# Kernel tuning notes

Measured on AMD Instinct MI355X. Metric: run time of the kernel, lower is better.

The kernel has to match this reference:

```python
import jax, jax.numpy as jnp
import numpy as np

EPS = 1e-5

def layer_norm(x, g, b):
    mu = jnp.mean(x, axis=-1, keepdims=True)
    var = jnp.var(x, axis=-1, keepdims=True)
    return (x - mu) * jax.lax.rsqrt(var + EPS) * g + b

def rel_shift(x):
    # x: [N, H, T1, T2] with T2 = 2*T1 - 1 -> [N, H, T1, T1]
    N, H, T1, T2 = x.shape
    zp = jnp.zeros((N, H, T1, 1), dtype=x.dtype)
    xp = jnp.concatenate([zp, x], axis=-1).reshape(N, H, T2 + 1, T1)
    x = xp[:, :, 1:, :].reshape(N, H, T1, T2)
    return x[:, :, :, : T2 // 2 + 1]

def setup_inputs() -> dict:
    B, T, D, Hh = 8, 1024, 512, 8
    dk = D // Hh
    P = 2 * T - 1
    key = jax.random.key(0)
    ks = jax.random.split(key, 12)
    s = 0.02
    return {
        "q": jax.random.normal(ks[0], (B, T, D), jnp.float32),
        "k": jax.random.normal(ks[1], (B, T, D), jnp.float32),
        "v": jax.random.normal(ks[2], (B, T, D), jnp.float32),
        "pos_emb": jax.random.normal(ks[3], (1, P, D), jnp.float32),
        "mask": jnp.ones((B, T, T), jnp.int32),
        "ln_q_g": jnp.ones((D,), jnp.float32), "ln_q_b": jnp.zeros((D,), jnp.float32),
        "ln_k_g": jnp.ones((D,), jnp.float32), "ln_k_b": jnp.zeros((D,), jnp.float32),
        "ln_v_g": jnp.ones((D,), jnp.float32), "ln_v_b": jnp.zeros((D,), jnp.float32),
        "w_q": jax.random.normal(ks[4], (D, D), jnp.float32) * s,   # [out, in]
        "w_k": jax.random.normal(ks[5], (D, D), jnp.float32) * s,
        "w_v": jax.random.normal(ks[6], (D, D), jnp.float32) * s,
        "w_pos": jax.random.normal(ks[7], (D, D), jnp.float32) * s,
        "w_fc": jax.random.normal(ks[8], (D, D), jnp.float32) * s,
        "pos_bias_u": jax.random.normal(ks[9], (Hh, dk), jnp.float32) * s,
        "pos_bias_v": jax.random.normal(ks[10], (Hh, dk), jnp.float32) * s,
    }

def reference(q, k, v, pos_emb, mask, ln_q_g, ln_q_b, ln_k_g, ln_k_b, ln_v_g, ln_v_b,
              w_q, w_k, w_v, w_pos, w_fc, pos_bias_u, pos_bias_v):
    B, T, D = q.shape
    H, dk = pos_bias_u.shape
    scale = 1.0 / np.sqrt(dk).astype(np.float32)
    residual = q
    qn = layer_norm(q, ln_q_g, ln_q_b)
    kn = layer_norm(k, ln_k_g, ln_k_b)
    vn = layer_norm(v, ln_v_g, ln_v_b)
    # projections (torch Linear: x @ W^T), reshape to [B, H, T, dk]
    qh = (qn @ w_q.T).reshape(B, T, H, dk)                      # [B, T, H, dk]
    kh = (kn @ w_k.T).reshape(B, T, H, dk).transpose(0, 2, 1, 3)  # [B, H, T, dk]
    vh = (vn @ w_v.T).reshape(B, T, H, dk).transpose(0, 2, 1, 3)
    p = (pos_emb @ w_pos.T).reshape(pos_emb.shape[0], -1, H, dk).transpose(0, 2, 1, 3)  # [1, H, P, dk]
    q_u = (qh + pos_bias_u).transpose(0, 2, 1, 3)  # [B, H, T, dk]
    q_v = (qh + pos_bias_v).transpose(0, 2, 1, 3)
    matrix_ac = jnp.einsum('bhqd,bhkd->bhqk', q_u, kh)          # [B, H, T, T]
    matrix_bd = jnp.einsum('bhqd,nhpd->bhqp', q_v, p)           # [B, H, T, 2T-1]
    matrix_bd = rel_shift(matrix_bd)                             # [B, H, T, T]
    scores = (matrix_ac + matrix_bd) * scale
    m = (mask[:, None, :, :] == 0)                               # [B, 1, T, T]
    scores = jnp.where(m, -jnp.inf, scores)
    attn = jax.nn.softmax(scores, axis=-1)
    attn = jnp.where(m, 0.0, attn)
    out = jnp.einsum('bhqk,bhkd->bhqd', attn, vh)                # [B, H, T, dk]
    out = out.transpose(0, 2, 1, 3).reshape(B, T, H * dk)
    out = out @ w_fc.T + residual
    return out, attn
```

## Files before the change

kernel.cpp:

```cpp
#include <hip/hip_runtime.h>

constexpr int cT  = 1024;
constexpr int cD  = 512;
constexpr int cDK = 64;
constexpr int cP  = 2047;
constexpr int PBS = 1040;

typedef __attribute__((ext_vector_type(8))) short short8;
typedef __attribute__((ext_vector_type(4))) float floatx4;

#define MFMA16(a,b,c) __builtin_amdgcn_mfma_f32_16x16x32_bf16((a),(b),(c),0,0,0)
#define SWZ(i,j) ((j) ^ ((((i) >> 2) & 3) << 3))

__device__ __forceinline__ void bar_lds(){
  asm volatile("s_waitcnt lgkmcnt(0)\n\ts_barrier" ::: "memory");
}

__device__ __forceinline__ unsigned short f2bf(float f){
  union { float f; unsigned int u; } x; x.f = f;
  unsigned int r = x.u + 0x7fffu + ((x.u >> 16) & 1u);
  return (unsigned short)(r >> 16);
}
__device__ __forceinline__ float bf2f(unsigned short h){
  union { unsigned int u; float f; } x; x.u = ((unsigned int)h) << 16;
  return x.f;
}
__device__ __forceinline__ short8 ld8(const unsigned short* p){
  return *(const short8*)p;
}

struct LN3 { const float* x[3]; const float* g[3]; const float* b[3]; unsigned short* y[3]; };
__global__ void __launch_bounds__(256) ln3_kernel(LN3 a)
{
  __shared__ float red[8];
  const int z = blockIdx.y;
  const int half = threadIdx.x >> 7;
  const int r = blockIdx.x * 2 + half;
  const int tid = threadIdx.x & 127;
  const float* x = a.x[z]; const float* g = a.g[z]; const float* b = a.b[z];
  unsigned short* y = a.y[z];
  const float4 v = ((const float4*)(x + (size_t)r * cD))[tid];
  float s  = v.x + v.y + v.z + v.w;
  float sq = v.x * v.x + v.y * v.y + v.z * v.z + v.w * v.w;
  #pragma unroll
  for (int o = 32; o; o >>= 1){ s += __shfl_xor(s, o); sq += __shfl_xor(sq, o); }
  const int w = (threadIdx.x >> 6) & 1;
  if ((threadIdx.x & 63) == 0){ red[half * 4 + w * 2] = s; red[half * 4 + w * 2 + 1] = sq; }
  __syncthreads();
  s  = red[half * 4]     + red[half * 4 + 2];
  sq = red[half * 4 + 1] + red[half * 4 + 3];
  const float mu  = s * (1.0f / cD);
  const float var = sq * (1.0f / cD) - mu * mu;
  const float rs  = rsqrtf(var + 1e-5f);
  const int c = tid * 4;
  const float4 gv = *(const float4*)(g + c);
  const float4 bv = *(const float4*)(b + c);
  const unsigned int o0 = (unsigned int)f2bf((v.x - mu) * rs * gv.x + bv.x)
                        | ((unsigned int)f2bf((v.y - mu) * rs * gv.y + bv.y) << 16);
  const unsigned int o1 = (unsigned int)f2bf((v.z - mu) * rs * gv.z + bv.z)
                        | ((unsigned int)f2bf((v.w - mu) * rs * gv.w + bv.w) << 16);
  ((uint2*)(y + (size_t)r * cD))[tid] = make_uint2(o0, o1);
}

struct Ptr5 { const float* p[5]; };
__global__ void __launch_bounds__(256) cast5_kernel(Ptr5 s, unsigned short* __restrict__ d){
  const int idx = blockIdx.x * 256 + threadIdx.x;
  const int seg = idx >> 18, off = idx & 262143;
  d[idx] = f2bf(s.p[seg][off]);
}
__global__ void __launch_bounds__(256) cast1_kernel(const float* __restrict__ s,
    unsigned short* __restrict__ d, int n){
  const int idx = blockIdx.x * 256 + threadIdx.x;
  if (idx < n) d[idx] = f2bf(s[idx]);
}

__global__ void __launch_bounds__(256) maskbits_kernel(
    const int* __restrict__ mask, unsigned int* __restrict__ bm)
{
  const int row = blockIdx.x * 4 + (threadIdx.x >> 6);
  const int lane = threadIdx.x & 63;
  #pragma unroll
  for (int ii = 0; ii < 16; ii++){
    const int m = mask[(size_t)row * cT + ii * 64 + lane];
    const unsigned long long bal = __ballot(m != 0);
    if (lane == 0)       bm[row * 32 + ii * 2]     = (unsigned int)bal;
    else if (lane == 32) bm[row * 32 + ii * 2 + 1] = (unsigned int)(bal >> 32);
  }
}

__global__ void __launch_bounds__(256, 4) gemm512_kernel(
    const unsigned short* __restrict__ A0, const unsigned short* __restrict__ W0,
    int M, int mode, float scaleA, unsigned short* __restrict__ outb,
    float* __restrict__ outf, const float* __restrict__ residual,
    const float* __restrict__ addq)
{
  const int z = blockIdx.z;
  const unsigned short* A = A0 + (size_t)z * 4194304;
  const unsigned short* W = W0 + (size_t)z * 262144;
  unsigned short* outz = outb ? outb + (size_t)z * 4194304 : outb;
  const float sA = (z == 0) ? scaleA : 1.0f;
  const int n0 = blockIdx.x * 128, m0 = blockIdx.y * 128;
  const int wave = threadIdx.x >> 6, lane = threadIdx.x & 63;
  const int wr = wave >> 1, wc = wave & 1;
  const int l15 = lane & 15, lq = lane >> 4;
  const int mb = m0 + wr * 64, nb = n0 + wc * 64;
  floatx4 acc[4][4];
  #pragma unroll
  for (int i = 0; i < 4; i++)
    #pragma unroll
    for (int j = 0; j < 4; j++) acc[i][j] = (floatx4){0.f, 0.f, 0.f, 0.f};
  #pragma unroll 2
  for (int k0 = 0; k0 < 512; k0 += 32){
    short8 af[4], bf[4];
    #pragma unroll
    for (int i = 0; i < 4; i++){
      int row = mb + i * 16 + l15; if (row >= M) row = M - 1;
      af[i] = ld8(A + (size_t)row * 512 + k0 + lq * 8);
      const int col = nb + i * 16 + l15;
      bf[i] = ld8(W + (size_t)col * 512 + k0 + lq * 8);
    }
    #pragma unroll
    for (int i = 0; i < 4; i++)
      #pragma unroll
      for (int j = 0; j < 4; j++)
        acc[i][j] = MFMA16(af[i], bf[j], acc[i][j]);
  }
  #pragma unroll
  for (int i = 0; i < 4; i++){
    #pragma unroll
    for (int j = 0; j < 4; j++){
      #pragma unroll
      for (int r = 0; r < 4; r++){
        const int row = mb + i * 16 + lq * 4 + r;
        const int col = nb + j * 16 + l15;
        if (row >= M) continue;
        float val = acc[i][j][r];
        if (mode == 0 && z == 0 && addq) val += addq[col];
        val *= sA;
        if (mode == 0){
          const int bb = row >> 10, t = row & 1023, h = col >> 6, d = col & 63;
          outz[(((size_t)(bb * 8 + h) * 1024 + t) << 6) + d] = f2bf(val);
        } else if (mode == 1){
          const int h = col >> 6, d = col & 63;
          outz[(((size_t)h * 2047 + row) << 6) + d] = f2bf(val);
        } else {
          const size_t idx = (size_t)row * 512 + col;
          outf[idx] = val + residual[idx];
        }
      }
    }
  }
}

__global__ void __launch_bounds__(256) transpose_v_kernel(
    const unsigned short* __restrict__ vh, unsigned short* __restrict__ vt)
{
  __shared__ unsigned short tile[64][65];
  const int bh = blockIdx.x, t0 = blockIdx.y * 64;
  const unsigned short* src = vh + ((size_t)bh * cT + t0) * cDK;
  #pragma unroll
  for (int i = 0; i < 16; i++){
    const int idx = threadIdx.x + i * 256;
    tile[idx >> 6][idx & 63] = src[idx];
  }
  __syncthreads();
  unsigned short* dst = vt + (size_t)bh * cDK * cT + t0;
  #pragma unroll
  for (int i = 0; i < 16; i++){
    const int idx = threadIdx.x + i * 256;
    const int d = idx >> 6, t = idx & 63;
    dst[(size_t)d * cT + t] = tile[t][d];
  }
}

__global__ void __launch_bounds__(256) dot_bias_kernel(
    const unsigned short* __restrict__ X, const float* __restrict__ bias,
    const float* __restrict__ bias2, float* __restrict__ out,
    int rows, int hdiv, float scale)
{
  const int row = blockIdx.x * 4 + (threadIdx.x >> 6);
  const int lane = threadIdx.x & 63;
  if (row >= rows) return;
  const int h = (row / hdiv) & 7;
  float bv = bias[h * 64 + lane];
  if (bias2) bv -= bias2[h * 64 + lane];
  float s = bf2f(X[(size_t)row * 64 + lane]) * bv;
  #pragma unroll
  for (int o = 32; o; o >>= 1) s += __shfl_xor(s, o);
  if (lane == 0) out[row] = s * scale;
}

__global__ void __launch_bounds__(512, 4) attn_kernel(
    const unsigned short* __restrict__ qh, const unsigned short* __restrict__ kh,
    const unsigned short* __restrict__ vt, const unsigned short* __restrict__ pproj,
    const float* __restrict__ vbias, const unsigned int* __restrict__ bm,
    float* __restrict__ attn_out, unsigned short* __restrict__ out_h)
{
  __shared__ float sc[16 * cT];
  unsigned short* pbuf = (unsigned short*)sc;
  const int bh = blockIdx.x, b = bh >> 3, h = bh & 7;
  const int q0 = blockIdx.y * 16;
  const int wave = threadIdx.x >> 6, lane = threadIdx.x & 63;
  const int l15 = lane & 15, lq = lane >> 4;
  const unsigned short* Q  = qh + (size_t)bh * cT * cDK;
  const unsigned short* Kp = kh + (size_t)bh * cT * cDK;
  const unsigned short* Pt = pproj + (size_t)h * cP * cDK;
  const float* vb = vbias + (size_t)h * cP;

  const short8 qf0 = ld8(Q + (size_t)(q0 + l15) * cDK + lq * 8);
  const short8 qf1 = ld8(Q + (size_t)(q0 + l15) * cDK + 32 + lq * 8);

  {
    short8 k0a[8], k1a[8];
    #pragma unroll
    for (int t = 0; t < 8; t++){
      const int jt = wave + t * 8;
      k0a[t] = ld8(Kp + (size_t)(jt * 16 + l15) * cDK + lq * 8);
      k1a[t] = ld8(Kp + (size_t)(jt * 16 + l15) * cDK + 32 + lq * 8);
    }
    #pragma unroll
    for (int t = 0; t < 8; t++){
      const int jt = wave + t * 8;
      floatx4 acc = (floatx4){0.f, 0.f, 0.f, 0.f};
      acc = MFMA16(qf0, k0a[t], acc);
      acc = MFMA16(qf1, k1a[t], acc);
      const int jb = jt * 16 + l15;
      #pragma unroll
      for (int r = 0; r < 4; r++){
        const int i = lq * 4 + r;
        sc[i * cT + (jb ^ (lq << 3))] = acc[r];
      }
    }
  }
  bar_lds();

  const int w0 = (cT - 1) - q0 - 15;
  {
    short8 p0a[8], p1a[8];
    float vba[8];
    #pragma unroll
    for (int t = 0; t < 8; t++){
      const int c = (wave + t * 8) * 16 + l15;
      int prow = w0 + c; if (prow > cP - 1) prow = cP - 1;
      p0a[t] = ld8(Pt + (size_t)prow * cDK + lq * 8);
      p1a[t] = ld8(Pt + (size_t)prow * cDK + 32 + lq * 8);
      vba[t] = vb[prow];
    }
    #pragma unroll
    for (int t = 0; t < 8; t++){
      const int c = (wave + t * 8) * 16 + l15;
      floatx4 acc = (floatx4){0.f, 0.f, 0.f, 0.f};
      acc = MFMA16(qf0, p0a[t], acc);
      acc = MFMA16(qf1, p1a[t], acc);
      #pragma unroll
      for (int r = 0; r < 4; r++){
        const int i = lq * 4 + r;
        const int j = c - 15 + i;
        if (j >= 0 && j < cT) sc[i * cT + SWZ(i, j)] += acc[r] + vba[t];
      }
    }
  }
  if (wave == 0){
    const int c = 1024 + l15;
    int prow = w0 + c; if (prow > cP - 1) prow = cP - 1;
    const short8 pf0 = ld8(Pt + (size_t)prow * cDK + lq * 8);
    const short8 pf1 = ld8(Pt + (size_t)prow * cDK + 32 + lq * 8);
    const float vbv = vb[prow];
    floatx4 acc = (floatx4){0.f, 0.f, 0.f, 0.f};
    acc = MFMA16(qf0, pf0, acc);
    acc = MFMA16(qf1, pf1, acc);
    #pragma unroll
    for (int r = 0; r < 4; r++){
      const int i = lq * 4 + r;
      const int j = c - 15 + i;
      if (j >= 0 && j < cT) sc[i * cT + SWZ(i, j)] += acc[r] + vbv;
    }
  }
  bar_lds();

  const unsigned short* V = vt + (size_t)bh * cDK * cT;
  const int d0 = (wave & 3) * 16;
  const int kh2 = wave >> 2;
  short8 vfr[8], vfb[8];
  #pragma unroll
  for (int ks = 0; ks < 8; ks++){
    const int j0v = (kh2 * 16 + ks) * 32;
    vfr[ks] = ld8(V + (size_t)(d0 + l15) * cT + j0v + lq * 8);
  }

  #pragma unroll
  for (int p = 0; p < 2; p++){
    if (p == 1){
      #pragma unroll
      for (int ks = 0; ks < 8; ks++){
        const int j0v = (kh2 * 16 + ks + 8) * 32;
        vfb[ks] = ld8(V + (size_t)(d0 + l15) * cT + j0v + lq * 8);
      }
    }
    const int i = p * 8 + wave;
    const int qrow = q0 + i;
    const unsigned int* bmr = bm + ((size_t)b * cT + qrow) * 32;
    const int xr = ((i >> 2) & 3) << 3;
    float vals[16];
    float mx = -INFINITY;
    #pragma unroll
    for (int ii = 0; ii < 4; ii++){
      const int j0 = lane * 4 + ii * 256;
      const unsigned int mw = bmr[(lane >> 3) + ii * 8] >> (4 * (lane & 7));
      const floatx4 sv = *(const floatx4*)&sc[i * cT + (j0 ^ xr)];
      #pragma unroll
      for (int tt = 0; tt < 4; tt++){
        float s = sv[tt];
        if (((mw >> tt) & 1u) == 0u) s = -INFINITY;
        vals[ii * 4 + tt] = s;
        mx = fmaxf(mx, s);
      }
    }
    #pragma unroll
    for (int o = 32; o; o >>= 1) mx = fmaxf(mx, __shfl_xor(mx, o));
    float sum = 0.f;
    #pragma unroll
    for (int ii = 0; ii < 16; ii++){
      const float e = (vals[ii] == -INFINITY) ? 0.f : __expf(vals[ii] - mx);
      vals[ii] = e; sum += e;
    }
    #pragma unroll
    for (int o = 32; o; o >>= 1) sum += __shfl_xor(sum, o);
    const float ri = sum > 0.f ? 1.f / sum : 0.f;
    bar_lds();
    float* arow = attn_out + ((size_t)bh * cT + qrow) * cT;
    unsigned short* prow_lds = pbuf + (size_t)i * PBS;
    #pragma unroll
    for (int ii = 0; ii < 4; ii++){
      const int j0 = lane * 4 + ii * 256;
      floatx4 pv;
      #pragma unroll
      for (int tt = 0; tt < 4; tt++) pv[tt] = vals[ii * 4 + tt] * ri;
      __builtin_nontemporal_store(pv, (floatx4*)(arow + j0));
      const unsigned int wlo = (unsigned int)f2bf(pv[0]) | ((unsigned int)f2bf(pv[1]) << 16);
      const unsigned int whi = (unsigned int)f2bf(pv[2]) | ((unsigned int)f2bf(pv[3]) << 16);
      *(unsigned long long*)(prow_lds + j0) =
          (unsigned long long)wlo | ((unsigned long long)whi << 32);
    }
  }
  bar_lds();

  floatx4 acc = (floatx4){0.f, 0.f, 0.f, 0.f};
  #pragma unroll
  for (int ks = 0; ks < 8; ks++){
    const int j0 = (kh2 * 16 + ks) * 32;
    const short8 af = ld8(pbuf + l15 * PBS + j0 + lq * 8);
    acc = MFMA16(af, vfr[ks], acc);
  }
  #pragma unroll
  for (int ks = 8; ks < 16; ks++){
    const int j0 = (kh2 * 16 + ks) * 32;
    const short8 af = ld8(pbuf + l15 * PBS + j0 + lq * 8);
    acc = MFMA16(af, vfb[ks - 8], acc);
  }
  float* red4 = sc + 10240;
  if (kh2 == 1) *(floatx4*)(red4 + ((wave & 3) * 256 + lane * 4)) = acc;
  bar_lds();
  if (kh2 == 0){
    acc += *(const floatx4*)(red4 + ((wave & 3) * 256 + lane * 4));
    #pragma unroll
    for (int r = 0; r < 4; r++){
      const int i = lq * 4 + r;
      out_h[((size_t)b * cT + q0 + i) * cD + h * cDK + d0 + l15] = f2bf(acc[r]);
    }
  }
}

extern "C" void kernel_launch(void* const* d_in, const int* in_sizes, int n_in,
                              void* d_out, int out_size, void* d_ws, size_t ws_size,
                              hipStream_t stream)
{
  const float* q    = (const float*)d_in[0];
  const float* k    = (const float*)d_in[1];
  const float* v    = (const float*)d_in[2];
  const float* pe   = (const float*)d_in[3];
  const int*   mask = (const int*)d_in[4];
  const float* lnqg = (const float*)d_in[5];
  const float* lnqb = (const float*)d_in[6];
  const float* lnkg = (const float*)d_in[7];
  const float* lnkb = (const float*)d_in[8];
  const float* lnvg = (const float*)d_in[9];
  const float* lnvb = (const float*)d_in[10];
  const float* wq   = (const float*)d_in[11];
  const float* wk   = (const float*)d_in[12];
  const float* wv   = (const float*)d_in[13];
  const float* wpos = (const float*)d_in[14];
  const float* wfc  = (const float*)d_in[15];
  const float* pbu  = (const float*)d_in[16];
  const float* pbv  = (const float*)d_in[17];

  float* out_f  = (float*)d_out;
  float* attn_f = out_f + (size_t)8 * 1024 * 512;

  unsigned char* scr = (unsigned char*)attn_f;
  size_t soff = 0;
  auto salloc = [&](size_t bytes){ void* p = scr + soff; soff += (bytes + 255) & ~(size_t)255; return p; };
  unsigned short* qn   = (unsigned short*)salloc((size_t)8192 * 512 * 2);
  unsigned short* kn   = (unsigned short*)salloc((size_t)8192 * 512 * 2);
  unsigned short* vn   = (unsigned short*)salloc((size_t)8192 * 512 * 2);
  unsigned short* pe_b = (unsigned short*)salloc((size_t)2047 * 512 * 2);
  (void)kn; (void)vn;

  unsigned char* ws = (unsigned char*)d_ws;
  size_t off = 0;
  auto alloc = [&](size_t bytes){ void* p = ws + off; off += (bytes + 255) & ~(size_t)255; return p; };
  unsigned short* w5_b = (unsigned short*)alloc(5 * 512 * 512 * 2);
  unsigned short* qhb  = (unsigned short*)alloc((size_t)8192 * 512 * 2);
  unsigned short* khb  = (unsigned short*)alloc((size_t)8192 * 512 * 2);
  unsigned short* vhb  = (unsigned short*)alloc((size_t)8192 * 512 * 2);
  unsigned short* vtb  = (unsigned short*)alloc((size_t)8192 * 512 * 2);
  unsigned short* ppb  = (unsigned short*)alloc((size_t)8 * 2047 * 64 * 2);
  float*          vbias= (float*)alloc((size_t)8 * 2047 * 4);
  unsigned short* ohb  = (unsigned short*)alloc((size_t)8192 * 512 * 2);
  unsigned int*   bmask= (unsigned int*)alloc((size_t)8192 * 32 * 4);
  (void)ws_size; (void)n_in; (void)in_sizes; (void)out_size;

  Ptr5 c5; c5.p[0] = wq; c5.p[1] = wk; c5.p[2] = wv; c5.p[3] = wpos; c5.p[4] = wfc;
  cast5_kernel<<<5120, 256, 0, stream>>>(c5, w5_b);
  cast1_kernel<<<4094, 256, 0, stream>>>(pe, pe_b, 2047 * 512);
  maskbits_kernel<<<2048, 256, 0, stream>>>(mask, bmask);

  LN3 l3;
  l3.x[0] = q; l3.x[1] = k; l3.x[2] = v;
  l3.g[0] = lnqg; l3.g[1] = lnkg; l3.g[2] = lnvg;
  l3.b[0] = lnqb; l3.b[1] = lnkb; l3.b[2] = lnvb;
  l3.y[0] = qn; l3.y[1] = kn; l3.y[2] = vn;
  ln3_kernel<<<dim3(4096, 3), 256, 0, stream>>>(l3);

  gemm512_kernel<<<dim3(4, 64, 3), 256, 0, stream>>>(qn, w5_b, 8192, 0, 0.125f,
                                                     qhb, nullptr, nullptr, pbu);
  gemm512_kernel<<<dim3(4, 16, 1), 256, 0, stream>>>(pe_b, w5_b + 3 * 262144, 2047, 1, 1.0f,
                                                     ppb, nullptr, nullptr, nullptr);

  transpose_v_kernel<<<dim3(64, 16), 256, 0, stream>>>(vhb, vtb);

  dot_bias_kernel<<<4094, 256, 0, stream>>>(ppb, pbv, pbu, vbias, 16376, 2047, 0.125f);

  attn_kernel<<<dim3(64, 64), 512, 0, stream>>>(qhb, khb, vtb, ppb, vbias,
                                                bmask, attn_f, ohb);

  gemm512_kernel<<<dim3(4, 64, 1), 256, 0, stream>>>(ohb, w5_b + 4 * 262144, 8192, 2, 1.0f,
                                                     nullptr, out_f, q, nullptr);
}
```

Baseline: 671.5 us.

## Stage projection GEMM tiles through double-buffered LDS with direct global-to-LDS loads

The 512-K projection GEMM now copies 128x32 A and W tiles into swizzled, double-buffered shared memory with global_load_lds, instead of each wave loading its fragments straight from global memory. The next K-slice is fetched while MFMAs run on the current one, and the four waves share one copy of each tile, which cuts redundant global and L2 traffic. It adds a barrier per K-step. It also drops the row clamp for M, so the last tile of the 2047-row positional projection may read one row past the end of its input.

```diff
diff --git a/kernel.cpp b/kernel.cpp
--- a/kernel.cpp
+++ b/kernel.cpp
@@ -15,6 +15,9 @@
 __device__ __forceinline__ void bar_lds(){
   asm volatile("s_waitcnt lgkmcnt(0)\n\ts_barrier" ::: "memory");
 }
+__device__ __forceinline__ void bar_vm(){
+  asm volatile("s_waitcnt vmcnt(0)\n\ts_barrier" ::: "memory");
+}
 
 __device__ __forceinline__ unsigned short f2bf(float f){
   union { float f; unsigned int u; } x; x.f = f;
@@ -27,6 +30,11 @@
 }
 __device__ __forceinline__ short8 ld8(const unsigned short* p){
   return *(const short8*)p;
+}
+__device__ __forceinline__ void gl_lds16(const unsigned short* g, unsigned short* l){
+  __builtin_amdgcn_global_load_lds(
+      (const __attribute__((address_space(1))) unsigned int*)g,
+      (__attribute__((address_space(3))) unsigned int*)l, 16, 0, 0);
 }
 
 struct LN3 { const float* x[3]; const float* g[3]; const float* b[3]; unsigned short* y[3]; };
@@ -94,45 +102,66 @@
     float* __restrict__ outf, const float* __restrict__ residual,
     const float* __restrict__ addq)
 {
+  __shared__ __align__(16) unsigned short lsA[2][4096];
+  __shared__ __align__(16) unsigned short lsB[2][4096];
   const int z = blockIdx.z;
   const unsigned short* A = A0 + (size_t)z * 4194304;
   const unsigned short* W = W0 + (size_t)z * 262144;
   unsigned short* outz = outb ? outb + (size_t)z * 4194304 : outb;
   const float sA = (z == 0) ? scaleA : 1.0f;
   const int n0 = blockIdx.x * 128, m0 = blockIdx.y * 128;
-  const int wave = threadIdx.x >> 6, lane = threadIdx.x & 63;
+  const int tid = threadIdx.x;
+  const int wave = tid >> 6, lane = tid & 63;
   const int wr = wave >> 1, wc = wave & 1;
   const int l15 = lane & 15, lq = lane >> 4;
-  const int mb = m0 + wr * 64, nb = n0 + wc * 64;
+  const int srow = tid >> 2;
+  const int scol = ((tid & 3) ^ ((tid >> 3) & 3)) * 8;
+  const int xr4  = (l15 >> 1) & 3;
+
+  auto STAGE = [&](int k0, int buf){
+    #pragma unroll
+    for (int s = 0; s < 2; s++){
+      gl_lds16(A + (size_t)(m0 + s * 64 + srow) * 512 + k0 + scol,
+               &lsA[buf][s * 2048 + wave * 512]);
+      gl_lds16(W + (size_t)(n0 + s * 64 + srow) * 512 + k0 + scol,
+               &lsB[buf][s * 2048 + wave * 512]);
+    }
+  };
+
   floatx4 acc[4][4];
   #pragma unroll
   for (int i = 0; i < 4; i++)
     #pragma unroll
     for (int j = 0; j < 4; j++) acc[i][j] = (floatx4){0.f, 0.f, 0.f, 0.f};
+
+  STAGE(0, 0);
+  bar_vm();
   #pragma unroll 2
-  for (int k0 = 0; k0 < 512; k0 += 32){
+  for (int ks = 0; ks < 16; ks++){
+    const int cur = ks & 1;
+    if (ks < 15) STAGE((ks + 1) * 32, cur ^ 1);
     short8 af[4], bf[4];
     #pragma unroll
     for (int i = 0; i < 4; i++){
-      int row = mb + i * 16 + l15; if (row >= M) row = M - 1;
-      af[i] = ld8(A + (size_t)row * 512 + k0 + lq * 8);
-      const int col = nb + i * 16 + l15;
-      bf[i] = ld8(W + (size_t)col * 512 + k0 + lq * 8);
+      af[i] = *(const short8*)&lsA[cur][(wr * 64 + i * 16 + l15) * 32 + ((lq ^ xr4) * 8)];
+      bf[i] = *(const short8*)&lsB[cur][(wc * 64 + i * 16 + l15) * 32 + ((lq ^ xr4) * 8)];
     }
     #pragma unroll
     for (int i = 0; i < 4; i++)
       #pragma unroll
       for (int j = 0; j < 4; j++)
         acc[i][j] = MFMA16(af[i], bf[j], acc[i][j]);
-  }
+    bar_vm();
+  }
+
   #pragma unroll
   for (int i = 0; i < 4; i++){
     #pragma unroll
     for (int j = 0; j < 4; j++){
       #pragma unroll
       for (int r = 0; r < 4; r++){
-        const int row = mb + i * 16 + lq * 4 + r;
-        const int col = nb + j * 16 + l15;
+        const int row = m0 + wr * 64 + i * 16 + lq * 4 + r;
+        const int col = n0 + wc * 64 + j * 16 + l15;
         if (row >= M) continue;
         float val = acc[i][j][r];
         if (mode == 0 && z == 0 && addq) val += addq[col];
```

After: 624.3 us. -7.0%, faster.
